# Performance work log

Measured on AMD Instinct MI355X. Metric: run time of the kernel, lower is better.

The kernel has to match this reference:

```python
import jax, jax.numpy as jnp
import numpy as np

HIDDEN = 256   # opt.hidden_dim
NHEADS = 8     # forced by .view(bs, nq, -1, 8)
LVLS = 4       # opt.num_feature_levels
NQ = 300       # opt.real_num_queries
BS = 2
LVL_HWS = [(128, 128), (64, 64), (32, 32), (16, 16)]  # ceil((1024/8)/2**l)
OUT = 7        # roi_align output_size
SR = 2         # fixed sampling_ratio (torchvision default -1 is adaptive/data-dependent)
_STARTS = np.cumsum([0] + [h * w for h, w in LVL_HWS]).tolist()


def setup_inputs():
    key = jax.random.key(0)
    ks = jax.random.split(key, 20)
    def rn(i, shape, s=1.0):
        return jax.random.normal(ks[i], shape, jnp.float32) * s
    total = _STARTS[-1]
    memory = rn(0, (BS, total, HIDDEN))
    tgt = rn(1, (BS, NQ, HIDDEN))
    cxcy = jax.random.uniform(ks[2], (BS, NQ, LVLS, 2), jnp.float32)
    ltrb = jax.random.uniform(ks[3], (BS, NQ, LVLS, 4), jnp.float32) * 0.2 + 0.02
    reference = jnp.concatenate([cxcy, ltrb], axis=-1)  # (bs, nq, lvls, 6)
    level_start_index = jnp.array(_STARTS[:LVLS], jnp.int32)
    C4 = HIDDEN // 4
    params = dict(
        p1_w=rn(4, (HIDDEN, C4), 0.05), p1_b=rn(5, (C4,), 0.05),
        p2_w1=rn(6, (C4 * OUT * OUT, 256), 0.02), p2_b1=rn(7, (256,), 0.02),
        p2_w2=rn(8, (256, 512), 0.02), p2_b2=rn(9, (512,), 0.02),
        p2_w3=rn(10, (512, 512), 0.02), p2_b3=rn(11, (512,), 0.02),
        p2_w4=rn(12, (512, NHEADS * 2), 0.02), p2_b4=rn(13, (NHEADS * 2,), 0.02),
        attn1_w=rn(14, (HIDDEN, HIDDEN * NHEADS), 0.02), attn1_b=rn(15, (HIDDEN * NHEADS,), 0.02),
        attn2_w=rn(16, (HIDDEN, 1), 0.05), attn2_b=rn(17, (1,), 0.05))
    return dict(tgt=tgt, memory=memory, reference=reference,
                level_start_index=level_start_index, **params)


def _roi_align(mem2d, boxes):
    """torchvision roi_align, aligned=True, output 7x7, sampling_ratio=SR.
    mem2d: (B,C,H,W); boxes: (B,nq,4) xyxy in feature coords -> (B,nq,C,7,7)."""
    B, C, H, W = mem2d.shape
    nq = boxes.shape[1]
    fl = mem2d.reshape(B, C, H * W)
    x1, y1, x2, y2 = boxes[..., 0], boxes[..., 1], boxes[..., 2], boxes[..., 3]
    sx, sy = x1 - 0.5, y1 - 0.5                      # aligned=True half-pixel offset
    bw, bh = (x2 - x1) / OUT, (y2 - y1) / OUT
    # sample positions: bin pw, subsample ix -> pw + (ix+0.5)/SR  (pw-major order)
    t = (jnp.arange(OUT, dtype=jnp.float32)[:, None]
         + (jnp.arange(SR, dtype=jnp.float32)[None, :] + 0.5) / SR).reshape(-1)  # (S,)
    S = OUT * SR
    xs = sx[..., None] + bw[..., None] * t           # (B,nq,S)
    ys = sy[..., None] + bh[..., None] * t
    yy = jnp.broadcast_to(ys[:, :, :, None], (B, nq, S, S)).reshape(B, -1)
    xx = jnp.broadcast_to(xs[:, :, None, :], (B, nq, S, S)).reshape(B, -1)
    valid = (yy >= -1.0) & (yy <= H) & (xx >= -1.0) & (xx <= W)
    yc = jnp.clip(yy, 0.0, H - 1.0)
    xc = jnp.clip(xx, 0.0, W - 1.0)
    y0 = jnp.clip(jnp.floor(yc), 0.0, H - 2.0)
    x0 = jnp.clip(jnp.floor(xc), 0.0, W - 2.0)
    ly, lx = yc - y0, xc - x0
    y0i, x0i = y0.astype(jnp.int32), x0.astype(jnp.int32)

    def g(yi, xi):
        return jnp.take_along_axis(fl, (yi * W + xi)[:, None, :], axis=2)  # (B,C,P)

    v = (((1 - ly) * (1 - lx))[:, None] * g(y0i, x0i)
         + ((1 - ly) * lx)[:, None] * g(y0i, x0i + 1)
         + (ly * (1 - lx))[:, None] * g(y0i + 1, x0i)
         + (ly * lx)[:, None] * g(y0i + 1, x0i + 1))
    v = v * valid[:, None, :].astype(v.dtype)
    v = v.reshape(B, C, nq, OUT, SR, OUT, SR).mean(axis=(4, 6))  # bin average
    return v.transpose(0, 2, 1, 3, 4)  # (B,nq,C,7,7)


def _grid_sample(feat, gx, gy):
    """F.grid_sample bilinear, padding_mode='zeros', align_corners=False.
    feat: (N,C,H,W); gx,gy: (N,P) in [-1,1] -> (N,C,P)."""
    N, C, H, W = feat.shape
    fl = feat.reshape(N, C, H * W)
    ix = ((gx + 1.0) * W - 1.0) * 0.5
    iy = ((gy + 1.0) * H - 1.0) * 0.5
    x0, y0 = jnp.floor(ix), jnp.floor(iy)
    lx, ly = ix - x0, iy - y0
    out = jnp.zeros((N, C, gx.shape[1]), feat.dtype)
    for dy, dx, w in ((0, 0, (1 - ly) * (1 - lx)), (0, 1, (1 - ly) * lx),
                      (1, 0, ly * (1 - lx)), (1, 1, ly * lx)):
        xi, yi = x0 + dx, y0 + dy
        m = (xi >= 0) & (xi < W) & (yi >= 0) & (yi < H)
        idx = (jnp.clip(yi, 0, H - 1) * W + jnp.clip(xi, 0, W - 1)).astype(jnp.int32)
        out = out + (w * m)[:, None, :] * jnp.take_along_axis(fl, idx[:, None, :], axis=2)
    return out


def _forward(tgt, memory, ref, p1_w, p1_b, p2_w1, p2_b1, p2_w2, p2_b2,
             p2_w3, p2_b3, p2_w4, p2_b4, attn1_w, attn1_b, attn2_w, attn2_b):
    B, nq = tgt.shape[0], tgt.shape[1]
    gate = jax.nn.sigmoid((tgt @ attn1_w + attn1_b).reshape(B, nq, NHEADS, HIDDEN))
    levels = []
    for lvi in range(LVLS):
        h, w = LVL_HWS[lvi]
        s = _STARTS[lvi]
        mem2d = memory[:, s:s + h * w, :].transpose(0, 2, 1).reshape(B, HIDDEN, h, w)
        r = ref[:, :, lvi]                            # (B,nq,6): cx,cy,l,t,r,b
        cx, cy = r[..., 0], r[..., 1]
        x1 = jnp.clip(cx - r[..., 2], 0.0, 1.0) * w
        y1 = jnp.clip(cy - r[..., 3], 0.0, 1.0) * h
        x2 = jnp.clip(cx + r[..., 4], 0.0, 1.0) * w
        y2 = jnp.clip(cy + r[..., 5], 0.0, 1.0) * h
        boxes = jnp.stack([x1, y1, x2, y2], axis=-1)
        roi = _roi_align(mem2d, boxes)                # (B,nq,C,7,7)
        # point1: 1x1 conv + ReLU, then point2 MLP -> per-head sample offsets
        p = jax.nn.relu(jnp.einsum('bqchw,cd->bqdhw', roi, p1_w) + p1_b[:, None, None])
        p = p.reshape(B, nq, -1)
        p = jax.nn.relu(p @ p2_w1 + p2_b1)
        p = jax.nn.relu(p @ p2_w2 + p2_b2)
        p = jax.nn.relu(p @ p2_w3 + p2_b3)
        pts = jnp.tanh(p @ p2_w4 + p2_b4).reshape(B * nq, NHEADS, 2)
        samp = _grid_sample(roi.reshape(B * nq, HIDDEN, OUT, OUT),
                            pts[..., 0], pts[..., 1])           # (B*nq,C,8)
        samp = samp.reshape(B, nq, HIDDEN, NHEADS).transpose(0, 1, 3, 2)  # (B,nq,8,C)
        levels.append(samp * gate)
    qe = jnp.stack(levels, axis=2).reshape(B, nq, LVLS * NHEADS, HIDDEN)
    wgt = jax.nn.softmax((qe @ attn2_w + attn2_b)[..., 0], axis=-1)  # (B,nq,lvls*heads)
    return (qe * wgt[..., None]).sum(axis=-2)  # (B,nq,C)


def reference(tgt, memory, reference, level_start_index, p1_w, p1_b,
              p2_w1, p2_b1, p2_w2, p2_b2, p2_w3, p2_b3, p2_w4, p2_b4,
              attn1_w, attn1_b, attn2_w, attn2_b):
    # level_start_index is consistent with the static LVL_HWS pyramid
    return _forward(tgt, memory, reference, p1_w, p1_b, p2_w1, p2_b1,
                    p2_w2, p2_b2, p2_w3, p2_b3, p2_w4, p2_b4,
                    attn1_w, attn1_b, attn2_w, attn2_b)
```

## Files before the change

kernel.cpp:

```cpp
#include <hip/hip_runtime.h>
#include <hip/hip_bf16.h>

#define NQ     300
#define NH     8
#define HID    256
#define NLVL   4
#define NCELL  49
#define TOTAL  21760

typedef unsigned short ushort_t;
typedef __attribute__((ext_vector_type(8))) short short8;
typedef __attribute__((ext_vector_type(4))) float floatx4;

__device__ __forceinline__ float bfbits2f(ushort_t u) {
    union { unsigned int i; float f; } x;
    x.i = ((unsigned int)u) << 16;
    return x.f;
}
__device__ __forceinline__ ushort_t f2bfbits(float v) {
    __hip_bfloat16 h = __float2bfloat16(v);
    return *(ushort_t*)&h;
}
__device__ __forceinline__ void split_bf(float v, ushort_t& hi, ushort_t& lo) {
    __hip_bfloat16 h = __float2bfloat16(v);
    hi = *(ushort_t*)&h;
    float hv = __bfloat162float(h);
    __hip_bfloat16 l = __float2bfloat16(v - hv);
    lo = *(ushort_t*)&l;
}

struct Box {
    float sx, sy, bw, bh, Wf;
    int W;
    const ushort_t* memb;
};

__device__ __forceinline__ void load_box(const float* __restrict__ refr,
                                         const ushort_t* __restrict__ mem16,
                                         int r, int lvl, int lane, Box& bx) {
    const int lvl_hw[4] = {128, 64, 32, 16};
    const int lvl_s[4]  = {0, 16384, 20480, 21504};
    const int b = r / NQ;
    bx.W  = lvl_hw[lvl];
    bx.Wf = (float)bx.W;
    const float* rp = refr + ((size_t)r * NLVL + lvl) * 6;
    float cx = rp[0], cy = rp[1];
    float dl = rp[2], dt = rp[3], dr = rp[4], db = rp[5];
    float x1 = fminf(fmaxf(cx - dl, 0.f), 1.f) * bx.Wf;
    float y1 = fminf(fmaxf(cy - dt, 0.f), 1.f) * bx.Wf;
    float x2 = fminf(fmaxf(cx + dr, 0.f), 1.f) * bx.Wf;
    float y2 = fminf(fmaxf(cy + db, 0.f), 1.f) * bx.Wf;
    bx.sx = x1 - 0.5f;
    bx.sy = y1 - 0.5f;
    bx.bw = (x2 - x1) * (1.f / 7.f);
    bx.bh = (y2 - y1) * (1.f / 7.f);
    bx.memb = mem16 + ((size_t)b * TOTAL + lvl_s[lvl]) * HID + lane * 4;
}

__device__ __forceinline__ void roi_cell(const Box& bx, int cell, float4& out) {
    const int ph = cell / 7, pw = cell % 7;
    float a0 = 0.f, a1 = 0.f, a2 = 0.f, a3 = 0.f;
#pragma unroll
    for (int sub = 0; sub < 4; ++sub) {
        const float tys = (float)ph + ((sub >> 1) + 0.5f) * 0.5f;
        const float txs = (float)pw + ((sub & 1) + 0.5f) * 0.5f;
        float yy = bx.sy + bx.bh * tys;
        float xx = bx.sx + bx.bw * txs;
        if (yy >= -1.f && yy <= bx.Wf && xx >= -1.f && xx <= bx.Wf) {
            float yc = fminf(fmaxf(yy, 0.f), bx.Wf - 1.f);
            float xc = fminf(fmaxf(xx, 0.f), bx.Wf - 1.f);
            float y0f = fminf(floorf(yc), bx.Wf - 2.f);
            float x0f = fminf(floorf(xc), bx.Wf - 2.f);
            float ly = yc - y0f, lx = xc - x0f;
            int y0 = (int)y0f, x0 = (int)x0f;
            const ushort_t* p00 = bx.memb + (size_t)(y0 * bx.W + x0) * HID;
            ushort4 u00 = *(const ushort4*)p00;
            ushort4 u01 = *(const ushort4*)(p00 + HID);
            ushort4 u10 = *(const ushort4*)(p00 + bx.W * HID);
            ushort4 u11 = *(const ushort4*)(p00 + bx.W * HID + HID);
            float w00 = (1.f - ly) * (1.f - lx), w01 = (1.f - ly) * lx;
            float w10 = ly * (1.f - lx), w11 = ly * lx;
            a0 += w00 * bfbits2f(u00.x) + w01 * bfbits2f(u01.x) + w10 * bfbits2f(u10.x) + w11 * bfbits2f(u11.x);
            a1 += w00 * bfbits2f(u00.y) + w01 * bfbits2f(u01.y) + w10 * bfbits2f(u10.y) + w11 * bfbits2f(u11.y);
            a2 += w00 * bfbits2f(u00.z) + w01 * bfbits2f(u01.z) + w10 * bfbits2f(u10.z) + w11 * bfbits2f(u11.z);
            a3 += w00 * bfbits2f(u00.w) + w01 * bfbits2f(u01.w) + w10 * bfbits2f(u10.w) + w11 * bfbits2f(u11.w);
        }
    }
    out.x = a0 * 0.25f; out.y = a1 * 0.25f; out.z = a2 * 0.25f; out.w = a3 * 0.25f;
}

__device__ __forceinline__ void tsplit_body(const float* __restrict__ W,
                                            ushort_t* __restrict__ TH,
                                            ushort_t* __restrict__ TL,
                                            int K, int N, int kb, int nb,
                                            int perm, int tid, float (*sm)[65]) {
    for (int e = tid; e < 64 * 64; e += 256) {
        int kk = e >> 6, nn = e & 63;
        int kp = kb + kk;
        int ks = perm ? ((kp & 63) * 49 + (kp >> 6)) : kp;
        sm[kk][nn] = W[(size_t)ks * N + nb + nn];
    }
    __syncthreads();
    for (int e = tid; e < 64 * 64; e += 256) {
        int nn = e >> 6, kk = e & 63;
        ushort_t h, l;
        split_bf(sm[kk][nn], h, l);
        size_t o = (size_t)(nb + nn) * K + kb + kk;
        TH[o] = h; TL[o] = l;
    }
}

__global__ __launch_bounds__(256) void k_prep(
    const float* __restrict__ tgt, ushort_t* __restrict__ tgtH, ushort_t* __restrict__ tgtL,
    const float* __restrict__ a1w, ushort_t* __restrict__ a1wTH, ushort_t* __restrict__ a1wTL,
    const float* __restrict__ w1, ushort_t* __restrict__ w1TH, ushort_t* __restrict__ w1TL,
    const float* __restrict__ w2, ushort_t* __restrict__ w2TH, ushort_t* __restrict__ w2TL,
    const float* __restrict__ w3, ushort_t* __restrict__ w3TH, ushort_t* __restrict__ w3TL,
    const float* __restrict__ p1w, ushort_t* __restrict__ p1wTH, ushort_t* __restrict__ p1wTL,
    const float* __restrict__ memory, ushort_t* __restrict__ mem16) {
    __shared__ float sm[64][65];
    const int tid = threadIdx.x;
    int b = blockIdx.x;
    if (b < 600) {
        int i = b * 256 + tid;
        ushort_t h, l;
        split_bf(tgt[i], h, l);
        tgtH[i] = h; tgtL[i] = l;
    } else if (b < 728) {
        b -= 600;
        tsplit_body(a1w, a1wTH, a1wTL, 256, 2048, (b % 4) * 64, (b / 4) * 64, 0, tid, sm);
    } else if (b < 924) {
        b -= 728;
        tsplit_body(w1, w1TH, w1TL, 3136, 256, (b % 49) * 64, (b / 49) * 64, 1, tid, sm);
    } else if (b < 956) {
        b -= 924;
        tsplit_body(w2, w2TH, w2TL, 256, 512, (b % 4) * 64, (b / 4) * 64, 0, tid, sm);
    } else if (b < 1020) {
        b -= 956;
        tsplit_body(w3, w3TH, w3TL, 512, 512, (b % 8) * 64, (b / 8) * 64, 0, tid, sm);
    } else if (b < 1024) {
        b -= 1020;
        tsplit_body(p1w, p1wTH, p1wTL, 256, 64, b * 64, 0, 0, tid, sm);
    } else {
        b -= 1024;
        size_t i = (size_t)b * 256 + tid;
        float4 v = ((const float4*)memory)[i];
        ushort4 o;
        o.x = f2bfbits(v.x); o.y = f2bfbits(v.y);
        o.z = f2bfbits(v.z); o.w = f2bfbits(v.w);
        ((ushort4*)mem16)[i] = o;
    }
}

template <int EPI, int AX>
__global__ __launch_bounds__(256) void k_gmfma(
    const ushort_t* __restrict__ AH, const ushort_t* __restrict__ AL,
    const ushort_t* __restrict__ WH, const ushort_t* __restrict__ WL,
    const float* __restrict__ bias, float* __restrict__ Cf,
    ushort_t* __restrict__ CH, ushort_t* __restrict__ CL,
    int M, int N, int K, int kchunk) {
    __shared__ ushort_t As[AX ? 1 : 2][64][40];
    __shared__ ushort_t Ws[2][64][40];

    const int tid = threadIdx.x;
    const int m0 = blockIdx.x * 64, n0 = blockIdx.y * 64;
    const int wv = tid >> 6, ln = tid & 63;
    const int row = tid >> 2, kc = tid & 3;
    const int gm = min(m0 + row, M - 1);
    const int gn = n0 + row;
    const int arow = wv * 16 + (ln & 15);
    const int koff = (ln >> 4) * 8;

    int kb = 0, ke = K;
    if (EPI == 3) {
        kb = blockIdx.z * kchunk;
        ke = min(K, kb + kchunk);
    }

    floatx4 acc[4];
#pragma unroll
    for (int t = 0; t < 4; ++t) acc[t] = (floatx4){0.f, 0.f, 0.f, 0.f};

    for (int k0 = kb; k0 < ke; k0 += 32) {
        *(uint4*)&As[0][row][kc * 8] = *(const uint4*)(AH + (size_t)gm * K + k0 + kc * 8);
        if constexpr (!AX)
            *(uint4*)&As[AX ? 0 : 1][row][kc * 8] = *(const uint4*)(AL + (size_t)gm * K + k0 + kc * 8);
        *(uint4*)&Ws[0][row][kc * 8] = *(const uint4*)(WH + (size_t)gn * K + k0 + kc * 8);
        *(uint4*)&Ws[1][row][kc * 8] = *(const uint4*)(WL + (size_t)gn * K + k0 + kc * 8);
        __syncthreads();

        short8 aH = *(short8*)&As[0][arow][koff];
        short8 aL = aH;
        if constexpr (!AX) aL = *(short8*)&As[AX ? 0 : 1][arow][koff];
#pragma unroll
        for (int t = 0; t < 4; ++t) {
            short8 wH = *(short8*)&Ws[0][t * 16 + (ln & 15)][koff];
            short8 wL = *(short8*)&Ws[1][t * 16 + (ln & 15)][koff];
            acc[t] = __builtin_amdgcn_mfma_f32_16x16x32_bf16(aH, wH, acc[t], 0, 0, 0);
            acc[t] = __builtin_amdgcn_mfma_f32_16x16x32_bf16(aH, wL, acc[t], 0, 0, 0);
            if constexpr (!AX)
                acc[t] = __builtin_amdgcn_mfma_f32_16x16x32_bf16(aL, wH, acc[t], 0, 0, 0);
        }
        __syncthreads();
    }

    float* Cpart = (EPI == 3) ? Cf + (size_t)blockIdx.z * M * N : Cf;
#pragma unroll
    for (int t = 0; t < 4; ++t) {
        int n = n0 + t * 16 + (ln & 15);
        float bv = (EPI == 3) ? 0.f : bias[n];
#pragma unroll
        for (int reg = 0; reg < 4; ++reg) {
            int m = m0 + wv * 16 + (ln >> 4) * 4 + reg;
            if (m < M) {
                float v = acc[t][reg] + bv;
                if (EPI == 0) {
                    v = fmaxf(v, 0.f);
                    ushort_t h, l;
                    split_bf(v, h, l);
                    CH[(size_t)m * N + n] = h;
                    CL[(size_t)m * N + n] = l;
                } else if (EPI == 1) {
                    Cf[(size_t)m * N + n] = fmaxf(v, 0.f);
                } else if (EPI == 2) {
                    Cf[(size_t)m * N + n] = 1.f / (1.f + expf(-v));
                } else {
                    Cpart[(size_t)m * N + n] = v;
                }
            }
        }
    }
}

__global__ __launch_bounds__(256) void k_h1red(
    const float* __restrict__ h1p, const float* __restrict__ b1,
    ushort_t* __restrict__ h1H, ushort_t* __restrict__ h1L) {
    const int idx = blockIdx.x * 256 + threadIdx.x;
    const int n = (idx * 4) & 255;
    float4 s = ((const float4*)h1p)[idx];
#pragma unroll
    for (int z = 1; z < 7; ++z) {
        float4 t = ((const float4*)(h1p + (size_t)z * 2400 * 256))[idx];
        s.x += t.x; s.y += t.y; s.z += t.z; s.w += t.w;
    }
    float4 bv = *(const float4*)(b1 + n);
    s.x = fmaxf(s.x + bv.x, 0.f);
    s.y = fmaxf(s.y + bv.y, 0.f);
    s.z = fmaxf(s.z + bv.z, 0.f);
    s.w = fmaxf(s.w + bv.w, 0.f);
    ushort4 H, L;
    split_bf(s.x, H.x, L.x);
    split_bf(s.y, H.y, L.y);
    split_bf(s.z, H.z, L.z);
    split_bf(s.w, H.w, L.w);
    ((ushort4*)h1H)[idx] = H;
    ((ushort4*)h1L)[idx] = L;
}

__global__ __launch_bounds__(256) void k_roi(
    const ushort_t* __restrict__ mem16, const float* __restrict__ refr,
    ushort_t* __restrict__ roi) {
    const int tid  = threadIdx.x;
    const int wave = tid >> 6, lane = tid & 63;
    const int lvl = blockIdx.x / 600;
    const int r   = blockIdx.x % 600;
    const int i2  = r * 4 + lvl;

    Box bx;
    load_box(refr, mem16, r, lvl, lane, bx);

    ushort_t* rbase = roi + (size_t)i2 * NCELL * HID;
    for (int cell = wave; cell < NCELL; cell += 4) {
        float4 o;
        roi_cell(bx, cell, o);
        ushort4 pk;
        pk.x = f2bfbits(o.x); pk.y = f2bfbits(o.y);
        pk.z = f2bfbits(o.z); pk.w = f2bfbits(o.w);
        *(ushort4*)&rbase[cell * HID + lane * 4] = pk;
    }
}

__global__ __launch_bounds__(256) void k_fuse(
    const ushort_t* __restrict__ roi, const float* __restrict__ h3,
    const float* __restrict__ w4, const float* __restrict__ b4,
    const float* __restrict__ gate, const float* __restrict__ w,
    const float* __restrict__ bias, float* __restrict__ out) {
    __shared__ float sm_qe[32 * HID];
    __shared__ float sm_pts[64];
    __shared__ float sm_hd[32][4];
    __shared__ float sm_l[32];
    __shared__ float sm_e[32];

    const int tid = threadIdx.x;
    const int r = blockIdx.x;

    float* sm_h3 = sm_qe;
    {
        const float4* src = (const float4*)(h3 + (size_t)r * 4 * 512);
        float4* dst = (float4*)sm_h3;
        for (int i = tid; i < 512; i += 256) dst[i] = src[i];
    }
    __syncthreads();

    {
        const int o = tid >> 2, s = tid & 3;
        const int row = o >> 4, col = o & 15;
        float part = 0.f;
        const int kb = s * 128;
        for (int k = kb; k < kb + 128; ++k)
            part += sm_h3[row * 512 + k] * w4[k * 16 + col];
        part += __shfl_down(part, 2);
        part += __shfl_down(part, 1);
        if (s == 0) sm_pts[row * 16 + col] = tanhf(part + b4[col]);
    }
    __syncthreads();

    if (tid < 32) {
        int lvl = tid >> 3, h = tid & 7;
        float gx = sm_pts[lvl * 16 + h * 2];
        float gy = sm_pts[lvl * 16 + h * 2 + 1];
        float ix = ((gx + 1.f) * 7.f - 1.f) * 0.5f;
        float iy = ((gy + 1.f) * 7.f - 1.f) * 0.5f;
        float x0f = floorf(ix), y0f = floorf(iy);
        sm_hd[tid][0] = x0f;
        sm_hd[tid][1] = y0f;
        sm_hd[tid][2] = ix - x0f;
        sm_hd[tid][3] = iy - y0f;
    }
    __syncthreads();

    const float* grow = gate + (size_t)r * 2048;
#pragma unroll
    for (int j = 0; j < 32; ++j) {
        int lvl = j >> 3, h = j & 7;
        const ushort_t* rbase = roi + ((size_t)r * 4 + lvl) * NCELL * HID;
        float x0f = sm_hd[j][0], y0f = sm_hd[j][1];
        float lx = sm_hd[j][2], ly = sm_hd[j][3];
        int x0 = (int)x0f, y0 = (int)y0f;
        float v = 0.f;
#pragma unroll
        for (int dy = 0; dy < 2; ++dy) {
            int yi = y0 + dy;
            if (yi < 0 || yi >= 7) continue;
            float wy = dy ? ly : 1.f - ly;
#pragma unroll
            for (int dx = 0; dx < 2; ++dx) {
                int xi = x0 + dx;
                if (xi < 0 || xi >= 7) continue;
                float wx = dx ? lx : 1.f - lx;
                v += wy * wx * bfbits2f(rbase[(yi * 7 + xi) * HID + tid]);
            }
        }
        sm_qe[j * HID + tid] = v * grow[h * HID + tid];
    }
    __syncthreads();

    const int j = tid >> 3, sub = tid & 7;
    float part = 0.f;
    const int cbase = sub * 32;
    for (int c = 0; c < 32; ++c) part += sm_qe[j * HID + cbase + c] * w[cbase + c];
    part += __shfl_down(part, 4);
    part += __shfl_down(part, 2);
    part += __shfl_down(part, 1);
    if (sub == 0) sm_l[j] = part + bias[0];
    __syncthreads();
    if (tid < 32) {
        float m = -1e30f;
        for (int i = 0; i < 32; ++i) m = fmaxf(m, sm_l[i]);
        sm_e[tid] = expf(sm_l[tid] - m);
    }
    __syncthreads();
    float denom = 0.f;
    for (int i = 0; i < 32; ++i) denom += sm_e[i];
    float inv = 1.f / denom;
    float acc = 0.f;
    for (int jj = 0; jj < 32; ++jj) acc += sm_qe[jj * HID + tid] * sm_e[jj];
    out[(size_t)r * HID + tid] = acc * inv;
}

extern "C" void kernel_launch(void* const* d_in, const int* in_sizes, int n_in,
                              void* d_out, int out_size, void* d_ws, size_t ws_size,
                              hipStream_t stream) {
    const float* tgt    = (const float*)d_in[0];
    const float* memory = (const float*)d_in[1];
    const float* refr   = (const float*)d_in[2];
    const float* p1w = (const float*)d_in[4];
    const float* p1b = (const float*)d_in[5];
    const float* w1  = (const float*)d_in[6];
    const float* b1  = (const float*)d_in[7];
    const float* w2  = (const float*)d_in[8];
    const float* b2  = (const float*)d_in[9];
    const float* w3  = (const float*)d_in[10];
    const float* b3  = (const float*)d_in[11];
    const float* w4  = (const float*)d_in[12];
    const float* b4  = (const float*)d_in[13];
    const float* a1w = (const float*)d_in[14];
    const float* a1b = (const float*)d_in[15];
    const float* a2w = (const float*)d_in[16];
    const float* a2b = (const float*)d_in[17];
    float* out = (float*)d_out;

    size_t off = 0;
    auto alloc = [&](size_t bytes) {
        void* p = (char*)d_ws + off;
        off += (bytes + 255) & ~(size_t)255;
        return p;
    };
    float*    gate  = (float*)alloc((size_t)600 * 2048 * 4);
    ushort_t* mem16 = (ushort_t*)alloc((size_t)2 * TOTAL * HID * 2);
    ushort_t* roi   = (ushort_t*)alloc((size_t)2400 * NCELL * HID * 2);
    ushort_t* pHb   = (ushort_t*)alloc((size_t)2400 * 3136 * 2);
    ushort_t* pLb   = (ushort_t*)alloc((size_t)2400 * 3136 * 2);
    float*    h1p   = (float*)alloc((size_t)7 * 2400 * 256 * 4);
    ushort_t* h1H   = (ushort_t*)alloc((size_t)2400 * 256 * 2);
    ushort_t* h1L   = (ushort_t*)alloc((size_t)2400 * 256 * 2);
    ushort_t* h2H   = (ushort_t*)alloc((size_t)2400 * 512 * 2);
    ushort_t* h2L   = (ushort_t*)alloc((size_t)2400 * 512 * 2);
    float*    h3    = (float*)alloc((size_t)2400 * 512 * 4);
    ushort_t* tgtH  = (ushort_t*)alloc((size_t)600 * 256 * 2);
    ushort_t* tgtL  = (ushort_t*)alloc((size_t)600 * 256 * 2);
    ushort_t* a1wTH = (ushort_t*)alloc((size_t)2048 * 256 * 2);
    ushort_t* a1wTL = (ushort_t*)alloc((size_t)2048 * 256 * 2);
    ushort_t* w1TH  = (ushort_t*)alloc((size_t)256 * 3136 * 2);
    ushort_t* w1TL  = (ushort_t*)alloc((size_t)256 * 3136 * 2);
    ushort_t* w2TH  = (ushort_t*)alloc((size_t)512 * 256 * 2);
    ushort_t* w2TL  = (ushort_t*)alloc((size_t)512 * 256 * 2);
    ushort_t* w3TH  = (ushort_t*)alloc((size_t)512 * 512 * 2);
    ushort_t* w3TL  = (ushort_t*)alloc((size_t)512 * 512 * 2);
    ushort_t* p1wTH = (ushort_t*)alloc((size_t)64 * 256 * 2);
    ushort_t* p1wTL = (ushort_t*)alloc((size_t)64 * 256 * 2);

    hipLaunchKernelGGL(k_prep, dim3(11904), dim3(256), 0, stream,
                       tgt, tgtH, tgtL, a1w, a1wTH, a1wTL,
                       w1, w1TH, w1TL, w2, w2TH, w2TL, w3, w3TH, w3TL,
                       p1w, p1wTH, p1wTL, memory, mem16);

    hipLaunchKernelGGL((k_gmfma<2, 0>), dim3(10, 32), dim3(256), 0, stream,
                       tgtH, tgtL, a1wTH, a1wTL, a1b, gate, (ushort_t*)0, (ushort_t*)0,
                       600, 2048, 256, 0);
    hipLaunchKernelGGL(k_roi, dim3(2400), dim3(256), 0, stream, mem16, refr, roi);
    hipLaunchKernelGGL((k_gmfma<0, 1>), dim3(1838, 1), dim3(256), 0, stream,
                       roi, (ushort_t*)0, p1wTH, p1wTL, p1b, (float*)0, pHb, pLb,
                       2400 * NCELL, 64, 256, 0);
    hipLaunchKernelGGL((k_gmfma<3, 0>), dim3(38, 4, 7), dim3(256), 0, stream,
                       pHb, pLb, w1TH, w1TL, (float*)0, h1p, (ushort_t*)0, (ushort_t*)0,
                       2400, 256, 3136, 448);
    hipLaunchKernelGGL(k_h1red, dim3(600), dim3(256), 0, stream, h1p, b1, h1H, h1L);
    hipLaunchKernelGGL((k_gmfma<0, 0>), dim3(38, 8), dim3(256), 0, stream,
                       h1H, h1L, w2TH, w2TL, b2, (float*)0, h2H, h2L, 2400, 512, 256, 0);
    hipLaunchKernelGGL((k_gmfma<1, 0>), dim3(38, 8), dim3(256), 0, stream,
                       h2H, h2L, w3TH, w3TL, b3, h3, (ushort_t*)0, (ushort_t*)0,
                       2400, 512, 512, 0);
    hipLaunchKernelGGL(k_fuse, dim3(600), dim3(256), 0, stream,
                       roi, h3, w4, b4, gate, a2w, a2b, out);
}
```

Measured before the change: 354.4 us.

## Sort ROI blocks by box center y for cache locality; store gate in bf16

Adds a per-level rank sort of the queries by batch and reference y-coordinate inside the prep kernel. k_roi then processes queries in an interleaved sorted order, so blocks that run at the same time read nearby rows of the feature map and get more L2 reuse. The sigmoid gate output is also stored as bf16 instead of fp32, which halves its write and read traffic. The costs are an O(n^2) rank computation in four prep blocks, an extra indirection per ROI block, and lower gate precision.

After: 382.3 us. +7.9%, slower.

```diff
diff --git a/kernel.cpp b/kernel.cpp
--- a/kernel.cpp
+++ b/kernel.cpp
@@ -117,32 +117,48 @@
     const float* __restrict__ w2, ushort_t* __restrict__ w2TH, ushort_t* __restrict__ w2TL,
     const float* __restrict__ w3, ushort_t* __restrict__ w3TH, ushort_t* __restrict__ w3TL,
     const float* __restrict__ p1w, ushort_t* __restrict__ p1wTH, ushort_t* __restrict__ p1wTL,
-    const float* __restrict__ memory, ushort_t* __restrict__ mem16) {
+    const float* __restrict__ memory, ushort_t* __restrict__ mem16,
+    const float* __restrict__ refr, int* __restrict__ qperm) {
     __shared__ float sm[64][65];
     const int tid = threadIdx.x;
     int b = blockIdx.x;
-    if (b < 600) {
-        int i = b * 256 + tid;
+    if (b < 4) {
+        const int lvl = b;
+        float* keys = (float*)sm;
+        for (int i = tid; i < 600; i += 256)
+            keys[i] = (float)(i / NQ) * 2.0f + refr[((size_t)i * 4 + lvl) * 6 + 1];
+        __syncthreads();
+        for (int i = tid; i < 600; i += 256) {
+            float ki = keys[i];
+            int rank = 0;
+            for (int j = 0; j < 600; ++j) {
+                float kj = keys[j];
+                rank += (kj < ki) || (kj == ki && j < i);
+            }
+            qperm[lvl * 600 + rank] = i;
+        }
+    } else if (b < 604) {
+        int i = (b - 4) * 256 + tid;
         ushort_t h, l;
         split_bf(tgt[i], h, l);
         tgtH[i] = h; tgtL[i] = l;
-    } else if (b < 728) {
-        b -= 600;
+    } else if (b < 732) {
+        b -= 604;
         tsplit_body(a1w, a1wTH, a1wTL, 256, 2048, (b % 4) * 64, (b / 4) * 64, 0, tid, sm);
-    } else if (b < 924) {
-        b -= 728;
+    } else if (b < 928) {
+        b -= 732;
         tsplit_body(w1, w1TH, w1TL, 3136, 256, (b % 49) * 64, (b / 49) * 64, 1, tid, sm);
-    } else if (b < 956) {
-        b -= 924;
+    } else if (b < 960) {
+        b -= 928;
         tsplit_body(w2, w2TH, w2TL, 256, 512, (b % 4) * 64, (b / 4) * 64, 0, tid, sm);
-    } else if (b < 1020) {
-        b -= 956;
+    } else if (b < 1024) {
+        b -= 960;
         tsplit_body(w3, w3TH, w3TL, 512, 512, (b % 8) * 64, (b / 8) * 64, 0, tid, sm);
-    } else if (b < 1024) {
-        b -= 1020;
+    } else if (b < 1028) {
+        b -= 1024;
         tsplit_body(p1w, p1wTH, p1wTL, 256, 64, b * 64, 0, 0, tid, sm);
     } else {
-        b -= 1024;
+        b -= 1028;
         size_t i = (size_t)b * 256 + tid;
         float4 v = ((const float4*)memory)[i];
         ushort4 o;
@@ -224,6 +240,8 @@
                     Cf[(size_t)m * N + n] = fmaxf(v, 0.f);
                 } else if (EPI == 2) {
                     Cf[(size_t)m * N + n] = 1.f / (1.f + expf(-v));
+                } else if (EPI == 4) {
+                    CH[(size_t)m * N + n] = f2bfbits(1.f / (1.f + expf(-v)));
                 } else {
                     Cpart[(size_t)m * N + n] = v;
                 }
@@ -259,11 +277,13 @@
 
 __global__ __launch_bounds__(256) void k_roi(
     const ushort_t* __restrict__ mem16, const float* __restrict__ refr,
-    ushort_t* __restrict__ roi) {
+    const int* __restrict__ qperm, ushort_t* __restrict__ roi) {
     const int tid  = threadIdx.x;
     const int wave = tid >> 6, lane = tid & 63;
     const int lvl = blockIdx.x / 600;
-    const int r   = blockIdx.x % 600;
+    const int jj  = blockIdx.x % 600;
+    const int rank = (jj & 7) * 75 + (jj >> 3);
+    const int r = qperm[lvl * 600 + rank];
     const int i2  = r * 4 + lvl;
 
     Box bx;
@@ -283,7 +303,7 @@
 __global__ __launch_bounds__(256) void k_fuse(
     const ushort_t* __restrict__ roi, const float* __restrict__ h3,
     const float* __restrict__ w4, const float* __restrict__ b4,
-    const float* __restrict__ gate, const float* __restrict__ w,
+    const ushort_t* __restrict__ gate, const float* __restrict__ w,
     const float* __restrict__ bias, float* __restrict__ out) {
     __shared__ float sm_qe[32 * HID];
     __shared__ float sm_pts[64];
@@ -329,7 +349,7 @@
     }
     __syncthreads();
 
-    const float* grow = gate + (size_t)r * 2048;
+    const ushort_t* grow = gate + (size_t)r * 2048;
 #pragma unroll
     for (int j = 0; j < 32; ++j) {
         int lvl = j >> 3, h = j & 7;
@@ -351,7 +371,7 @@
                 v += wy * wx * bfbits2f(rbase[(yi * 7 + xi) * HID + tid]);
             }
         }
-        sm_qe[j * HID + tid] = v * grow[h * HID + tid];
+        sm_qe[j * HID + tid] = v * bfbits2f(grow[h * HID + tid]);
     }
     __syncthreads();
 
@@ -406,7 +426,7 @@
         off += (bytes + 255) & ~(size_t)255;
         return p;
     };
-    float*    gate  = (float*)alloc((size_t)600 * 2048 * 4);
+    ushort_t* gate  = (ushort_t*)alloc((size_t)600 * 2048 * 2);
     ushort_t* mem16 = (ushort_t*)alloc((size_t)2 * TOTAL * HID * 2);
     ushort_t* roi   = (ushort_t*)alloc((size_t)2400 * NCELL * HID * 2);
     ushort_t* pHb   = (ushort_t*)alloc((size_t)2400 * 3136 * 2);
@@ -429,16 +449,17 @@
     ushort_t* w3TL  = (ushort_t*)alloc((size_t)512 * 512 * 2);
     ushort_t* p1wTH = (ushort_t*)alloc((size_t)64 * 256 * 2);
     ushort_t* p1wTL = (ushort_t*)alloc((size_t)64 * 256 * 2);
-
-    hipLaunchKernelGGL(k_prep, dim3(11904), dim3(256), 0, stream,
+    int*      qperm = (int*)alloc((size_t)4 * 600 * 4);
+
+    hipLaunchKernelGGL(k_prep, dim3(11908), dim3(256), 0, stream,
                        tgt, tgtH, tgtL, a1w, a1wTH, a1wTL,
                        w1, w1TH, w1TL, w2, w2TH, w2TL, w3, w3TH, w3TL,
-                       p1w, p1wTH, p1wTL, memory, mem16);
-
-    hipLaunchKernelGGL((k_gmfma<2, 0>), dim3(10, 32), dim3(256), 0, stream,
-                       tgtH, tgtL, a1wTH, a1wTL, a1b, gate, (ushort_t*)0, (ushort_t*)0,
+                       p1w, p1wTH, p1wTL, memory, mem16, refr, qperm);
+
+    hipLaunchKernelGGL((k_gmfma<4, 0>), dim3(10, 32), dim3(256), 0, stream,
+                       tgtH, tgtL, a1wTH, a1wTL, a1b, (float*)0, gate, (ushort_t*)0,
                        600, 2048, 256, 0);
-    hipLaunchKernelGGL(k_roi, dim3(2400), dim3(256), 0, stream, mem16, refr, roi);
+    hipLaunchKernelGGL(k_roi, dim3(2400), dim3(256), 0, stream, mem16, refr, qperm, roi);
     hipLaunchKernelGGL((k_gmfma<0, 1>), dim3(1838, 1), dim3(256), 0, stream,
                        roi, (ushort_t*)0, p1wTH, p1wTL, p1b, (float*)0, pHb, pLb,
                        2400 * NCELL, 64, 256, 0);
```
